# Kernel tuning notes

Measured on AMD Instinct MI355X. Metric: run time of the kernel, lower is better.

## Reference

```python
import jax, jax.numpy as jnp
import numpy as np

LEAKY = 0.1

def square_distance(src, dst):
    # src [B,N,3], dst [B,M,3] -> [B,N,M]
    d = -2.0 * jnp.einsum('bnc,bmc->bnm', src, dst)
    d = d + jnp.sum(src * src, -1)[:, :, None]
    d = d + jnp.sum(dst * dst, -1)[:, None, :]
    return d

def knn_point(k, xyz, new_xyz):
    # indices of k smallest distances (largest=False)
    d = square_distance(new_xyz, xyz)
    _, idx = jax.lax.top_k(-d, k)
    return idx  # [B,S,k]

def gather_group(points, idx):
    # points [B,N,C], idx [B,S,K] -> [B,S,K,C]  (index_points_group)
    B, S, K = idx.shape
    flat = idx.reshape(B, S * K)
    out = jnp.take_along_axis(points, flat[:, :, None], axis=1)
    return out.reshape(B, S, K, points.shape[-1])

def leaky(x):
    return jnp.where(x >= 0, x, LEAKY * x)


def setup_inputs() -> dict:
    key = jax.random.key(0)
    ks = jax.random.split(key, 8)
    B, N, D = 2, 8192, 64
    H, O = 128, 64
    return {
        'xyz1': jax.random.normal(ks[0], (B, 3, N), jnp.float32),
        'xyz2': jax.random.normal(ks[1], (B, 3, N), jnp.float32),
        'flow1': jax.random.normal(ks[2], (B, 3, N), jnp.float32) * 0.1,
        'feat2': jax.random.normal(ks[3], (B, D, N), jnp.float32),
        'W1': jax.random.normal(ks[4], (H, 3 + D), jnp.float32) * (1.0 / np.sqrt(3 + D)),
        'b1': jnp.zeros((H,), jnp.float32),
        'W2': jax.random.normal(ks[5], (O, H), jnp.float32) * (1.0 / np.sqrt(H)),
        'b2': jnp.zeros((O,), jnp.float32),
        'nsample': 16,
    }


def reference(xyz1, xyz2, flow1, feat2, W1, b1, W2, b2, nsample):
    # to [B,N,3] / [B,N,D]
    xyz1p = jnp.transpose(xyz1, (0, 2, 1))
    xyz2p = jnp.transpose(xyz2, (0, 2, 1))
    flow1p = jnp.transpose(flow1, (0, 2, 1))
    feat2p = jnp.transpose(feat2, (0, 2, 1))
    B, N, _ = xyz1p.shape

    # ---- PointWarping: 3-NN inverse-distance interpolation of flow1 onto xyz2 ----
    xyz1_to_2 = xyz1p + flow1p                                   # [B,N,3]
    knn3 = knn_point(3, xyz1_to_2, xyz2p)                        # [B,N,3]
    g = gather_group(xyz1_to_2, knn3) - xyz2p[:, :, None, :]     # [B,N,3,3]
    dist = jnp.maximum(jnp.sqrt(jnp.sum(g * g, -1)), 1e-10)      # [B,N,3]
    inv = 1.0 / dist
    w = inv / jnp.sum(inv, axis=2, keepdims=True)                # [B,N,3]
    grouped_flow = gather_group(flow1p, knn3)                    # [B,N,3,3]
    flow2 = jnp.sum(w[..., None] * grouped_flow, axis=2)         # [B,N,3]
    warped_xyz2 = xyz2p - flow2                                  # [B,N,3]

    # ---- group_query: K-NN cost-volume grouping of frame-2 features around xyz1 ----
    idx = knn_point(nsample, warped_xyz2, xyz1p)                 # [B,N,K]
    grouped_xyz = gather_group(warped_xyz2, idx)                 # [B,N,K,3]
    grouped_xyz_norm = grouped_xyz - xyz1p[:, :, None, :]
    grouped_feat = gather_group(feat2p, idx)                     # [B,N,K,D]
    new_points = jnp.concatenate([grouped_xyz_norm, grouped_feat], axis=-1)  # [B,N,K,3+D]

    # ---- per-point Conv1d MLP (1x1 conv == linear) + LeakyReLU, max over K ----
    h = leaky(jnp.einsum('bnkc,hc->bnkh', new_points, W1) + b1)  # [B,N,K,H]
    h = leaky(jnp.einsum('bnkh,oh->bnko', h, W2) + b2)           # [B,N,K,O]
    out = jnp.max(h, axis=2)                                     # [B,N,O]
    return (jnp.transpose(out, (0, 2, 1)), jnp.transpose(warped_xyz2, (0, 2, 1)))
```

## Files before the change

### kernel.cpp

```cpp
#include <hip/hip_runtime.h>
#include <math.h>

#define NPTS 8192
#define NB 2
#define DF 64
#define HID 128
#define OUTC 64
#define KNN 16

typedef __attribute__((ext_vector_type(8))) short short8v;
typedef __attribute__((ext_vector_type(4))) float f32x4;

__device__ __forceinline__ unsigned short f2bf(float f) {
  unsigned int u = __float_as_uint(f);
  u += 0x7fffu + ((u >> 16) & 1u);
  return (unsigned short)(u >> 16);
}

__device__ __forceinline__ float readlane_f(float v, int l) {
  return __uint_as_float(__builtin_amdgcn_readlane(__float_as_uint(v), l));
}
__device__ __forceinline__ int readlane_i(int v, int l) {
  return (int)__builtin_amdgcn_readlane((unsigned)v, l);
}

__global__ void k_prep(const float* __restrict__ xyz1, const float* __restrict__ xyz2,
                       const float* __restrict__ flow1,
                       float4* __restrict__ A, float4* __restrict__ Bq, float4* __restrict__ Qx) {
  int t = blockIdx.x * 256 + threadIdx.x;
  int b = t >> 13, n = t & (NPTS - 1);
  size_t base = (size_t)b * 3 * NPTS + n;
  float x1 = xyz1[base], y1 = xyz1[base + NPTS], z1 = xyz1[base + 2 * NPTS];
  float fx = flow1[base], fy = flow1[base + NPTS], fz = flow1[base + 2 * NPTS];
  float sx = x1 + fx, sy = y1 + fy, sz = z1 + fz;
  A[t]  = make_float4(sx, sy, sz, 0.f);
  Bq[t] = make_float4(x1, y1, z1, 0.f);
  float x2 = xyz2[base], y2 = xyz2[base + NPTS], z2 = xyz2[base + 2 * NPTS];
  Qx[t] = make_float4(x2, y2, z2, 0.f);
}

__global__ void k_feat_T(const float* __restrict__ feat2, float* __restrict__ F) {
  __shared__ float t[64][65];
  int b = blockIdx.y;
  int n0 = blockIdx.x * 64;
  int l = threadIdx.x & 63, w = threadIdx.x >> 6;
#pragma unroll
  for (int it = 0; it < 16; ++it) {
    int dd = w + it * 4;
    t[dd][l] = feat2[((size_t)b * DF + dd) * NPTS + n0 + l];
  }
  __syncthreads();
#pragma unroll
  for (int it = 0; it < 16; ++it) {
    int nn = w + it * 4;
    F[((size_t)b * NPTS + n0 + nn) * DF + l] = t[l][nn];
  }
}

__global__ void k_w1t(const float* __restrict__ W1, float* __restrict__ W1T) {
  int t = blockIdx.x * 256 + threadIdx.x;
  if (t >= 67 * 128) return;
  int c = t >> 7, h = t & 127;
  W1T[t] = W1[h * 67 + c];
}

__global__ void k_w2frag(const float* __restrict__ W2, unsigned short* __restrict__ W2f) {
  int t = blockIdx.x * 256 + threadIdx.x;
  if (t >= 1024) return;
  int frag = t >> 6, lane = t & 63;
  int step = frag >> 2, ot = frag & 3;
  int col = ot * 16 + (lane & 15);
  int k0 = step * 32 + (lane >> 4) * 8;
#pragma unroll
  for (int j = 0; j < 8; ++j)
    W2f[t * 8 + j] = f2bf(W2[col * HID + k0 + j]);
}

__global__ void k_hfeat(const float* __restrict__ F, const float* __restrict__ W1T,
                        const float* __restrict__ b1, float* __restrict__ Hfeat) {
  int tid = threadIdx.x;
  int pt = blockIdx.x * 2 + (tid >> 7);
  int h = tid & 127;
  const float* fr = F + (size_t)pt * DF;
  float a = b1[h];
#pragma unroll
  for (int c = 0; c < DF; ++c) a = fmaf(fr[c], W1T[(3 + c) * HID + h], a);
  Hfeat[(size_t)pt * HID + h] = a;
}

__device__ __forceinline__ void bitonic64(float& d, int& i, int lane) {
#pragma unroll
  for (int k2 = 2; k2 <= 64; k2 <<= 1) {
#pragma unroll
    for (int j2 = k2 >> 1; j2 > 0; j2 >>= 1) {
      float pd = __shfl_xor(d, j2);
      int   pi = __shfl_xor(i, j2);
      bool swp = (pd < d) || (pd == d && pi < i);
      bool take = (((lane & k2) == 0) == ((lane & j2) == 0)) ? swp : !swp;
      d = take ? pd : d;
      i = take ? pi : i;
    }
  }
}

template<int K>
__device__ __forceinline__ void wave_insert(unsigned long long m, float d, int pid,
                                            int lane, float& ld, int& li, float& cap, int& ci) {
  do {
    int c = __ffsll(m) - 1; m &= m - 1;
    float bd = readlane_f(d, c); int bi = readlane_i(pid, c);
    bool pred = (ld > bd) || (ld == bd && li > bi);
    unsigned long long pm = __ballot(pred);
    float sld = __shfl_up(ld, 1);
    int   sli = __shfl_up(li, 1);
    bool pp = lane ? ((pm >> (lane - 1)) & 1ull) : false;
    ld = pred ? (pp ? sld : bd) : ld;
    li = pred ? (pp ? sli : bi) : li;
    cap = readlane_f(ld, K - 1); ci = readlane_i(li, K - 1);
    if (m) m &= __ballot((d < cap) || (d == cap && pid < ci));
  } while (m);
}

template<int K>
__global__ void __launch_bounds__(256) k_knn_lds(const float4* __restrict__ db,
                                                 const float4* __restrict__ qry,
                                                 int* __restrict__ outIdx) {
  __shared__ float4 tile[1024];
  int bk = blockIdx.x;
  int b = bk >> 10;
  int wave = threadIdx.x >> 6, lane = threadIdx.x & 63;
  int qb = bk * 8 + wave * 2;
  float4 Q0 = qry[qb], Q1 = qry[qb + 1];
  const float4* dbase = db + (size_t)b * NPTS;

#pragma unroll
  for (int i = 0; i < 4; ++i) tile[threadIdx.x + i * 256] = dbase[threadIdx.x + i * 256];
  __syncthreads();

  float ld0, ld1; int li0 = lane, li1 = lane;
  {
    float4 p = tile[lane];
    float dx = Q0.x - p.x, dy = Q0.y - p.y, dz = Q0.z - p.z;
    ld0 = fmaf(dx, dx, fmaf(dy, dy, dz * dz));
    dx = Q1.x - p.x; dy = Q1.y - p.y; dz = Q1.z - p.z;
    ld1 = fmaf(dx, dx, fmaf(dy, dy, dz * dz));
  }
  bitonic64(ld0, li0, lane);
  bitonic64(ld1, li1, lane);
  float cap0 = readlane_f(ld0, K - 1), cap1 = readlane_f(ld1, K - 1);
  int ci0 = readlane_i(li0, K - 1), ci1 = readlane_i(li1, K - 1);

  for (int chunk = 0; chunk < 8; ++chunk) {
    if (chunk) {
      __syncthreads();
#pragma unroll
      for (int i = 0; i < 4; ++i)
        tile[threadIdx.x + i * 256] = dbase[chunk * 1024 + threadIdx.x + i * 256];
      __syncthreads();
    }
    for (int it = (chunk == 0) ? 1 : 0; it < 16; ++it) {
      int j = chunk * 1024 + it * 64 + lane;
      float4 p = tile[it * 64 + lane];
      float ax = Q0.x - p.x, ay = Q0.y - p.y, az = Q0.z - p.z;
      float d0 = fmaf(ax, ax, fmaf(ay, ay, az * az));
      float bx = Q1.x - p.x, by = Q1.y - p.y, bz = Q1.z - p.z;
      float d1 = fmaf(bx, bx, fmaf(by, by, bz * bz));

      unsigned long long m0 = __ballot((d0 < cap0) || (d0 == cap0 && j < ci0));
      if (m0) wave_insert<K>(m0, d0, j, lane, ld0, li0, cap0, ci0);
      unsigned long long m1 = __ballot((d1 < cap1) || (d1 == cap1 && j < ci1));
      if (m1) wave_insert<K>(m1, d1, j, lane, ld1, li1, cap1, ci1);
    }
  }
  if (lane < K) {
    outIdx[(qb + 0) * K + lane] = li0;
    outIdx[(qb + 1) * K + lane] = li1;
  }
}

__global__ void k_warp_finish(const int* __restrict__ idx3,
                              const float4* __restrict__ A, const float4* __restrict__ Qx,
                              const float* __restrict__ flow1, float* __restrict__ out1,
                              float4* __restrict__ C) {
  int qg = blockIdx.x * 256 + threadIdx.x;
  int b = qg >> 13, n = qg & (NPTS - 1);
  int idx[3];
#pragma unroll
  for (int r = 0; r < 3; ++r) idx[r] = idx3[qg * 3 + r];
  float4 q = Qx[qg];
  float ivd[3];
  float s = 0.f;
#pragma unroll
  for (int r = 0; r < 3; ++r) {
    float4 p = A[b * NPTS + idx[r]];
    float gx = p.x - q.x, gy = p.y - q.y, gz = p.z - q.z;
    float dist = sqrtf(gx * gx + gy * gy + gz * gz);
    dist = fmaxf(dist, 1e-10f);
    ivd[r] = 1.0f / dist;
    s += ivd[r];
  }
  float w0 = ivd[0] / s, w1 = ivd[1] / s, w2 = ivd[2] / s;
  size_t fb = (size_t)b * 3 * NPTS;
  float f2x = w0 * flow1[fb + idx[0]]            + w1 * flow1[fb + idx[1]]            + w2 * flow1[fb + idx[2]];
  float f2y = w0 * flow1[fb + NPTS + idx[0]]     + w1 * flow1[fb + NPTS + idx[1]]     + w2 * flow1[fb + NPTS + idx[2]];
  float f2z = w0 * flow1[fb + 2 * NPTS + idx[0]] + w1 * flow1[fb + 2 * NPTS + idx[1]] + w2 * flow1[fb + 2 * NPTS + idx[2]];
  float wx = q.x - f2x, wy = q.y - f2y, wz = q.z - f2z;
  out1[fb + n] = wx;
  out1[fb + NPTS + n] = wy;
  out1[fb + 2 * NPTS + n] = wz;
  C[qg] = make_float4(wx, wy, wz, 0.f);
}

__global__ void __launch_bounds__(256) k_mlp3(const int* __restrict__ Didx, const float4* __restrict__ C,
                                              const float4* __restrict__ Bq, const float* __restrict__ Hfeat,
                                              const float* __restrict__ W1T, const unsigned short* __restrict__ W2f,
                                              const float* __restrict__ b2, float* __restrict__ out0) {
  int lane = threadIdx.x & 63;
  int wg = blockIdx.x * 4 + (threadIdx.x >> 6);
  int fr = lane & 15, fq = lane >> 4;

  short8v Bfr[16];
  const short8v* wf = (const short8v*)W2f;
#pragma unroll
  for (int i = 0; i < 16; ++i) Bfr[i] = wf[i * 64 + lane];
  float b2v0 = b2[fr], b2v1 = b2[16 + fr], b2v2 = b2[32 + fr], b2v3 = b2[48 + fr];

  for (int iq = 0; iq < 4; ++iq) {
    int q = wg * 4 + iq;
    int b = q >> 13, n = q & (NPTS - 1);
    int idx = Didx[q * KNN + fr];
    float4 wp = C[b * NPTS + idx];
    float4 qp = Bq[q];
    float dx = wp.x - qp.x, dy = wp.y - qp.y, dz = wp.z - qp.z;
    const float* hf = Hfeat + ((size_t)(b * NPTS + idx)) * HID;

    f32x4 acc0 = {b2v0, b2v0, b2v0, b2v0};
    f32x4 acc1 = {b2v1, b2v1, b2v1, b2v1};
    f32x4 acc2 = {b2v2, b2v2, b2v2, b2v2};
    f32x4 acc3 = {b2v3, b2v3, b2v3, b2v3};

#pragma unroll
    for (int step = 0; step < 4; ++step) {
      int k0 = step * 32 + fq * 8;
      float4 ha = *(const float4*)(hf + k0);
      float4 hb = *(const float4*)(hf + k0 + 4);
      float4 wx0 = *(const float4*)(W1T + k0);
      float4 wx1 = *(const float4*)(W1T + k0 + 4);
      float4 wy0 = *(const float4*)(W1T + HID + k0);
      float4 wy1 = *(const float4*)(W1T + HID + k0 + 4);
      float4 wz0 = *(const float4*)(W1T + 2 * HID + k0);
      float4 wz1 = *(const float4*)(W1T + 2 * HID + k0 + 4);
      float h[8];
      h[0] = fmaf(dx, wx0.x, fmaf(dy, wy0.x, fmaf(dz, wz0.x, ha.x)));
      h[1] = fmaf(dx, wx0.y, fmaf(dy, wy0.y, fmaf(dz, wz0.y, ha.y)));
      h[2] = fmaf(dx, wx0.z, fmaf(dy, wy0.z, fmaf(dz, wz0.z, ha.z)));
      h[3] = fmaf(dx, wx0.w, fmaf(dy, wy0.w, fmaf(dz, wz0.w, ha.w)));
      h[4] = fmaf(dx, wx1.x, fmaf(dy, wy1.x, fmaf(dz, wz1.x, hb.x)));
      h[5] = fmaf(dx, wx1.y, fmaf(dy, wy1.y, fmaf(dz, wz1.y, hb.y)));
      h[6] = fmaf(dx, wx1.z, fmaf(dy, wy1.z, fmaf(dz, wz1.z, hb.z)));
      h[7] = fmaf(dx, wx1.w, fmaf(dy, wy1.w, fmaf(dz, wz1.w, hb.w)));
      short8v a;
#pragma unroll
      for (int j = 0; j < 8; ++j) {
        float v = h[j];
        v = v >= 0.f ? v : 0.1f * v;
        a[j] = (short)f2bf(v);
      }
      acc0 = __builtin_amdgcn_mfma_f32_16x16x32_bf16(a, Bfr[step * 4 + 0], acc0, 0, 0, 0);
      acc1 = __builtin_amdgcn_mfma_f32_16x16x32_bf16(a, Bfr[step * 4 + 1], acc1, 0, 0, 0);
      acc2 = __builtin_amdgcn_mfma_f32_16x16x32_bf16(a, Bfr[step * 4 + 2], acc2, 0, 0, 0);
      acc3 = __builtin_amdgcn_mfma_f32_16x16x32_bf16(a, Bfr[step * 4 + 3], acc3, 0, 0, 0);
    }

    int ob = (b * OUTC) * NPTS + n;
#pragma unroll
    for (int ot = 0; ot < 4; ++ot) {
      f32x4 ac = ot == 0 ? acc0 : (ot == 1 ? acc1 : (ot == 2 ? acc2 : acc3));
      float m = fmaxf(fmaxf(ac[0], ac[1]), fmaxf(ac[2], ac[3]));
      m = fmaxf(m, __shfl_xor(m, 16));
      m = fmaxf(m, __shfl_xor(m, 32));
      m = m >= 0.f ? m : 0.1f * m;
      if (lane < 16) out0[ob + (ot * 16 + lane) * NPTS] = m;
    }
  }
}

extern "C" void kernel_launch(void* const* d_in, const int* in_sizes, int n_in,
                              void* d_out, int out_size, void* d_ws, size_t ws_size,
                              hipStream_t stream) {
  const float* xyz1  = (const float*)d_in[0];
  const float* xyz2  = (const float*)d_in[1];
  const float* flow1 = (const float*)d_in[2];
  const float* feat2 = (const float*)d_in[3];
  const float* W1    = (const float*)d_in[4];
  const float* b1    = (const float*)d_in[5];
  const float* W2    = (const float*)d_in[6];
  const float* b2    = (const float*)d_in[7];
  float* out0 = (float*)d_out;
  float* out1 = out0 + (size_t)NB * OUTC * NPTS;

  float* w = (float*)d_ws;
  float4* A     = (float4*)(w);
  float4* Bq    = (float4*)(w + 65536);
  float4* Qx    = (float4*)(w + 131072);
  float4* Cw    = (float4*)(w + 196608);
  float*  F     = w + 262144;
  float*  Hfeat = w + 1310720;
  float*  W1T   = w + 3407872;
  int*    idx3  = (int*)(w + 3424256);
  int*    Didx  = (int*)(w + 3473408);
  unsigned short* W2f = (unsigned short*)(w + 3735552);

  k_prep<<<64, 256, 0, stream>>>(xyz1, xyz2, flow1, A, Bq, Qx);
  k_feat_T<<<dim3(128, 2), 256, 0, stream>>>(feat2, F);
  k_w1t<<<34, 256, 0, stream>>>(W1, W1T);
  k_w2frag<<<4, 256, 0, stream>>>(W2, W2f);
  k_hfeat<<<NB * NPTS / 2, 256, 0, stream>>>(F, W1T, b1, Hfeat);

  k_knn_lds<3><<<2048, 256, 0, stream>>>(A, Qx, idx3);
  k_warp_finish<<<64, 256, 0, stream>>>(idx3, A, Qx, flow1, out1, Cw);
  k_knn_lds<16><<<2048, 256, 0, stream>>>(Cw, Bq, Didx);
  k_mlp3<<<1024, 256, 0, stream>>>(Didx, Cw, Bq, Hfeat, W1T, W2f, b2, out0);
}
```

Before: 261.7 us.

## Buffer KNN candidates in LDS and batch-merge with bitonic sort

Replaces the per-candidate serial wave insertion in the KNN kernel with per-query LDS candidate buffers. Admitted candidates are compacted by ballot rank and merged into the sorted list by a bitonic merge only when a buffer fills. The aim is to cut the long serial readlane/ballot loop per admitted point, especially for K=16. The cost is extra LDS, bitonic sorting work per flush, and a threshold that goes stale between flushes, so more candidates get admitted.

```diff
diff --git a/kernel.cpp b/kernel.cpp
--- a/kernel.cpp
+++ b/kernel.cpp
@@ -19,9 +19,6 @@
 
 __device__ __forceinline__ float readlane_f(float v, int l) {
   return __uint_as_float(__builtin_amdgcn_readlane(__float_as_uint(v), l));
-}
-__device__ __forceinline__ int readlane_i(int v, int l) {
-  return (int)__builtin_amdgcn_readlane((unsigned)v, l);
 }
 
 __global__ void k_prep(const float* __restrict__ xyz1, const float* __restrict__ xyz2,
@@ -104,34 +101,44 @@
 }
 
 template<int K>
-__device__ __forceinline__ void wave_insert(unsigned long long m, float d, int pid,
-                                            int lane, float& ld, int& li, float& cap, int& ci) {
-  do {
-    int c = __ffsll(m) - 1; m &= m - 1;
-    float bd = readlane_f(d, c); int bi = readlane_i(pid, c);
-    bool pred = (ld > bd) || (ld == bd && li > bi);
-    unsigned long long pm = __ballot(pred);
-    float sld = __shfl_up(ld, 1);
-    int   sli = __shfl_up(li, 1);
-    bool pp = lane ? ((pm >> (lane - 1)) & 1ull) : false;
-    ld = pred ? (pp ? sld : bd) : ld;
-    li = pred ? (pp ? sli : bi) : li;
-    cap = readlane_f(ld, K - 1); ci = readlane_i(li, K - 1);
-    if (m) m &= __ballot((d < cap) || (d == cap && pid < ci));
-  } while (m);
+__device__ __forceinline__ void flush_merge(const float* bufD, const int* bufJ, int base,
+                                            int cnt, int lane,
+                                            float& ld, int& li, float& cap) {
+  float bd = (lane < cnt) ? bufD[base + lane] : __builtin_inff();
+  int   bj = (lane < cnt) ? bufJ[base + lane] : 0x7fffffff;
+  bitonic64(bd, bj, lane);
+  float rd = __shfl_xor(bd, 63);
+  int   rj = __shfl_xor(bj, 63);
+  bool tk = (rd < ld) || (rd == ld && rj < li);
+  float nd = tk ? rd : ld;
+  int   nj = tk ? rj : li;
+#pragma unroll
+  for (int j2 = 32; j2 >= 1; j2 >>= 1) {
+    float pd = __shfl_xor(nd, j2);
+    int   pi = __shfl_xor(nj, j2);
+    bool sm = (pd < nd) || (pd == nd && pi < nj);
+    bool take = ((lane & j2) == 0) ? sm : !sm;
+    nd = take ? pd : nd;
+    nj = take ? pi : nj;
+  }
+  ld = nd; li = nj;
+  cap = readlane_f(ld, K - 1);
 }
 
 template<int K>
-__global__ void __launch_bounds__(256) k_knn_lds(const float4* __restrict__ db,
+__global__ void __launch_bounds__(256) k_knn_buf(const float4* __restrict__ db,
                                                  const float4* __restrict__ qry,
                                                  int* __restrict__ outIdx) {
   __shared__ float4 tile[1024];
+  __shared__ float bufD[512];
+  __shared__ int   bufJ[512];
   int bk = blockIdx.x;
   int b = bk >> 10;
   int wave = threadIdx.x >> 6, lane = threadIdx.x & 63;
   int qb = bk * 8 + wave * 2;
   float4 Q0 = qry[qb], Q1 = qry[qb + 1];
   const float4* dbase = db + (size_t)b * NPTS;
+  int base0 = (wave * 2 + 0) * 64, base1 = (wave * 2 + 1) * 64;
 
 #pragma unroll
   for (int i = 0; i < 4; ++i) tile[threadIdx.x + i * 256] = dbase[threadIdx.x + i * 256];
@@ -148,7 +155,7 @@
   bitonic64(ld0, li0, lane);
   bitonic64(ld1, li1, lane);
   float cap0 = readlane_f(ld0, K - 1), cap1 = readlane_f(ld1, K - 1);
-  int ci0 = readlane_i(li0, K - 1), ci1 = readlane_i(li1, K - 1);
+  int cnt0 = 0, cnt1 = 0;
 
   for (int chunk = 0; chunk < 8; ++chunk) {
     if (chunk) {
@@ -166,12 +173,35 @@
       float bx = Q1.x - p.x, by = Q1.y - p.y, bz = Q1.z - p.z;
       float d1 = fmaf(bx, bx, fmaf(by, by, bz * bz));
 
-      unsigned long long m0 = __ballot((d0 < cap0) || (d0 == cap0 && j < ci0));
-      if (m0) wave_insert<K>(m0, d0, j, lane, ld0, li0, cap0, ci0);
-      unsigned long long m1 = __ballot((d1 < cap1) || (d1 == cap1 && j < ci1));
-      if (m1) wave_insert<K>(m1, d1, j, lane, ld1, li1, cap1, ci1);
-    }
-  }
+      bool adm0 = d0 <= cap0;
+      unsigned long long m0 = __ballot(adm0);
+      if (m0) {
+        int pc = __popcll(m0);
+        if (cnt0 + pc > 64) {
+          flush_merge<K>(bufD, bufJ, base0, cnt0, lane, ld0, li0, cap0);
+          cnt0 = 0;
+        }
+        int rank = __popcll(m0 & ((1ull << lane) - 1ull));
+        if (adm0) { bufD[base0 + cnt0 + rank] = d0; bufJ[base0 + cnt0 + rank] = j; }
+        cnt0 += pc;
+      }
+      bool adm1 = d1 <= cap1;
+      unsigned long long m1 = __ballot(adm1);
+      if (m1) {
+        int pc = __popcll(m1);
+        if (cnt1 + pc > 64) {
+          flush_merge<K>(bufD, bufJ, base1, cnt1, lane, ld1, li1, cap1);
+          cnt1 = 0;
+        }
+        int rank = __popcll(m1 & ((1ull << lane) - 1ull));
+        if (adm1) { bufD[base1 + cnt1 + rank] = d1; bufJ[base1 + cnt1 + rank] = j; }
+        cnt1 += pc;
+      }
+    }
+  }
+  if (cnt0) flush_merge<K>(bufD, bufJ, base0, cnt0, lane, ld0, li0, cap0);
+  if (cnt1) flush_merge<K>(bufD, bufJ, base1, cnt1, lane, ld1, li1, cap1);
+
   if (lane < K) {
     outIdx[(qb + 0) * K + lane] = li0;
     outIdx[(qb + 1) * K + lane] = li1;
@@ -317,8 +347,8 @@
   k_w2frag<<<4, 256, 0, stream>>>(W2, W2f);
   k_hfeat<<<NB * NPTS / 2, 256, 0, stream>>>(F, W1T, b1, Hfeat);
 
-  k_knn_lds<3><<<2048, 256, 0, stream>>>(A, Qx, idx3);
+  k_knn_buf<3><<<2048, 256, 0, stream>>>(A, Qx, idx3);
   k_warp_finish<<<64, 256, 0, stream>>>(idx3, A, Qx, flow1, out1, Cw);
-  k_knn_lds<16><<<2048, 256, 0, stream>>>(Cw, Bq, Didx);
+  k_knn_buf<16><<<2048, 256, 0, stream>>>(Cw, Bq, Didx);
   k_mlp3<<<1024, 256, 0, stream>>>(Didx, Cw, Bq, Hfeat, W1T, W2f, b2, out0);
 }
```

Result: slower. 299.8 us (+14.6%).
